# Performance work log

Measured on AMD Instinct MI355X. Metric: run time of the kernel, lower is better.

The kernel has to match this reference:

```python
import jax, jax.numpy as jnp
import numpy as np

B, T, N = 8, 168, 1024
FD, FS, FF = 16, 32, 8
DL, DG, HE, E = 128, 128, 4, 16384
BN = B * N


def _lstm_last(x, Wih, Whh, bih, bhh):
    # x: (BN, T, FD); PyTorch gate order i, f, g, o
    h0 = jnp.zeros((x.shape[0], Whh.shape[1]), x.dtype)
    def step(carry, xt):
        h, c = carry
        g = xt @ Wih.T + h @ Whh.T + bih + bhh
        i, f, gg, o = jnp.split(g, 4, axis=-1)
        c = jax.nn.sigmoid(f) * c + jax.nn.sigmoid(i) * jnp.tanh(gg)
        h = jax.nn.sigmoid(o) * jnp.tanh(c)
        return (h, c), None
    (h, _), _ = jax.lax.scan(step, (h0, h0), jnp.swapaxes(x, 0, 1))
    return h


def _ln(x, g, b):
    mu = x.mean(-1, keepdims=True)
    v = ((x - mu) ** 2).mean(-1, keepdims=True)
    return (x - mu) / jnp.sqrt(v + 1e-5) * g + b


def _gat(x, src, dst, ea, W, a_src, a_dst, a_edge, We, bias):
    # PyG GATConv: concat=False (mean over heads), edge_dim=1, LeakyReLU(0.2)
    xl = (x @ W.T).reshape(BN, HE, -1)                 # (BN, H, C)
    as_ = jnp.sum(xl * a_src, -1)                      # (BN, H)
    ad_ = jnp.sum(xl * a_dst, -1)
    ep = (ea @ We.T).reshape(-1, HE, xl.shape[-1])     # (Eb, H, C)
    ae_ = jnp.sum(ep * a_edge, -1)                     # (Eb, H)
    alpha = jax.nn.leaky_relu(as_[src] + ad_[dst] + ae_, 0.2)
    amax = jax.ops.segment_max(alpha, dst, num_segments=BN)
    ex = jnp.exp(alpha - amax[dst])
    den = jax.ops.segment_sum(ex, dst, num_segments=BN)
    w = ex / den[dst]                                  # softmax over incoming edges
    out = jax.ops.segment_sum(w[:, :, None] * xl[src], dst, num_segments=BN)
    return out.mean(axis=1) + bias


def _forward(fl, edge_index):
    (dyn, fcst, sta, ew,
     lWih, lWhh, lbih, lbhh, sW, sb, fW, fb, uW, ub,
     g0W, g0as, g0ad, g0ae, g0We, g0b,
     g1W, g1as, g1ad, g1ae, g1We, g1b,
     n0g, n0b, n1g, n1b, oW, ob) = fl
    x = jnp.transpose(dyn, (0, 2, 1, 3)).reshape(BN, T, FD)
    z = _lstm_last(x, lWih, lWhh, lbih, lbhh)
    s = jax.nn.relu(sta.reshape(BN, -1) @ sW.T + sb)
    f = jax.nn.relu(fcst.reshape(BN, -1) @ fW.T + fb)
    h = jax.nn.relu(jnp.concatenate([z, s, f], -1) @ uW.T + ub)
    # batch the graph: B disjoint copies with node offsets
    off = (jnp.arange(B) * N)[:, None]
    src = (edge_index[0][None] + off).reshape(-1)
    dst = (edge_index[1][None] + off).reshape(-1)
    ea = jnp.tile(ew.reshape(-1, 1), (B, 1))           # (B*E, 1)
    # PyG GATConv default add_self_loops=True, fill_value='mean' of incoming edge attrs
    deg = jax.ops.segment_sum(jnp.ones_like(ea), dst, num_segments=BN)
    loop_ea = jax.ops.segment_sum(ea, dst, num_segments=BN) / jnp.maximum(deg, 1.0)
    loops = jnp.arange(BN)
    src = jnp.concatenate([src, loops])
    dst = jnp.concatenate([dst, loops])
    ea = jnp.concatenate([ea, loop_ea], 0)
    # hop 0: relu on delta (not last hop), residual (res_proj=None since DL==DG), LayerNorm
    d0 = jax.nn.relu(_gat(h, src, dst, ea, g0W, g0as, g0ad, g0ae, g0We, g0b))
    h = _ln(h + d0, n0g, n0b)
    # hop 1: last hop, no relu on delta
    d1 = _gat(h, src, dst, ea, g1W, g1as, g1ad, g1ae, g1We, g1b)
    h = _ln(h + d1, n1g, n1b)
    return (h @ oW.T + ob).reshape(B, N)


def setup_inputs():
    key = jax.random.key(0)
    ks = iter(jax.random.split(key, 48))
    def rn(shape, s=0.08):
        return jax.random.normal(next(ks), shape, jnp.float32) * s
    HO = HE * DG  # heads * out_channels
    return dict(
        dynamic_features=rn((B, T, N, FD), 1.0),
        forecast_features=rn((B, N, FF), 1.0),
        static_features=rn((B, N, FS), 1.0),
        edge_index=jax.random.randint(next(ks), (2, E), 0, N),
        edge_weight=jax.random.uniform(next(ks), (E,), jnp.float32),
        lstm_Wih=rn((4 * DL, FD)), lstm_Whh=rn((4 * DL, DL)),
        lstm_bih=rn((4 * DL,)), lstm_bhh=rn((4 * DL,)),
        static_W=rn((DL, FS)), static_b=rn((DL,)),
        fcst_W=rn((DL, FF)), fcst_b=rn((DL,)),
        fusion_W=rn((DL, 3 * DL)), fusion_b=rn((DL,)),
        gat0_W=rn((HO, DL)), gat0_att_src=rn((1, HE, DG)), gat0_att_dst=rn((1, HE, DG)),
        gat0_att_edge=rn((1, HE, DG)), gat0_We=rn((HO, 1)), gat0_bias=rn((DG,)),
        gat1_W=rn((HO, DG)), gat1_att_src=rn((1, HE, DG)), gat1_att_dst=rn((1, HE, DG)),
        gat1_att_edge=rn((1, HE, DG)), gat1_We=rn((HO, 1)), gat1_bias=rn((DG,)),
        ln0_g=jnp.ones((DG,), jnp.float32), ln0_b=jnp.zeros((DG,), jnp.float32),
        ln1_g=jnp.ones((DG,), jnp.float32), ln1_b=jnp.zeros((DG,), jnp.float32),
        out_W=rn((1, DG)), out_b=rn((1,)),
    )


def reference(dynamic_features, forecast_features, static_features, edge_weight,
              lstm_Wih, lstm_Whh, lstm_bih, lstm_bhh, static_W, static_b,
              fcst_W, fcst_b, fusion_W, fusion_b,
              gat0_W, gat0_att_src, gat0_att_dst, gat0_att_edge, gat0_We, gat0_bias,
              gat1_W, gat1_att_src, gat1_att_dst, gat1_att_edge, gat1_We, gat1_bias,
              ln0_g, ln0_b, ln1_g, ln1_b, out_W, out_b, edge_index):
    fl = (dynamic_features, forecast_features, static_features, edge_weight,
          lstm_Wih, lstm_Whh, lstm_bih, lstm_bhh, static_W, static_b,
          fcst_W, fcst_b, fusion_W, fusion_b,
          gat0_W, gat0_att_src, gat0_att_dst, gat0_att_edge, gat0_We, gat0_bias,
          gat1_W, gat1_att_src, gat1_att_dst, gat1_att_edge, gat1_We, gat1_bias,
          ln0_g, ln0_b, ln1_g, ln1_b, out_W, out_b)
    return _forward(fl, edge_index)
```

## Files before the change

### kernel.cpp

```cpp
#include <hip/hip_runtime.h>
#include <hip/hip_bf16.h>
#include <stdint.h>

#define BB 8
#define TT 168
#define NN 1024
#define BN_ 8192
#define FD_ 16
#define EE 16384

typedef short short8 __attribute__((ext_vector_type(8)));
typedef __bf16 bf16x8 __attribute__((ext_vector_type(8)));
typedef float f32x4 __attribute__((ext_vector_type(4)));

#if __has_builtin(__builtin_amdgcn_exp2f)
#define EXP2(x) __builtin_amdgcn_exp2f(x)
#else
#define EXP2(x) exp2f(x)
#endif
#if __has_builtin(__builtin_amdgcn_rcpf)
#define RCPF(x) __builtin_amdgcn_rcpf(x)
#else
#define RCPF(x) (1.f / (x))
#endif
#define L2E 1.4426950408889634f
#define T2E 2.8853900817779268f

static __device__ __forceinline__ float b2f(ushort s) {
    unsigned u = ((unsigned)s) << 16;
    return __builtin_bit_cast(float, u);
}
static __device__ __forceinline__ float b2f_lo(unsigned u) {
    return __builtin_bit_cast(float, u << 16);
}
static __device__ __forceinline__ float b2f_hi(unsigned u) {
    return __builtin_bit_cast(float, u & 0xffff0000u);
}
static __device__ __forceinline__ ushort f2b(float f) {
    unsigned u = __builtin_bit_cast(unsigned, f);
    unsigned lsb = (u >> 16) & 1u;
    u += 0x7fffu + lsb;
    return (ushort)(u >> 16);
}
static __device__ __forceinline__ ushort f2b_fast(float f) {
    unsigned u = __builtin_bit_cast(unsigned, f);
    return (ushort)((u + 0x8000u) >> 16);
}
static __device__ __forceinline__ f32x4 mfma16(short8 a, short8 b, f32x4 c) {
    return __builtin_amdgcn_mfma_f32_16x16x32_bf16(
        __builtin_bit_cast(bf16x8, a), __builtin_bit_cast(bf16x8, b), c, 0, 0, 0);
}

#define O_WIH 0
#define O_WHH 8192
#define O_STA 73728
#define O_FCS 335872
#define O_SW  401408
#define O_FW  405504
#define O_UW  406528
#define O_G0W 455680
#define O_G1W 521216
#define O_END 586752

__global__ void cast_kernel(const float* __restrict__ Wih, const float* __restrict__ Whh,
                            const float* __restrict__ sta, const float* __restrict__ fcst,
                            const float* __restrict__ sW, const float* __restrict__ fW,
                            const float* __restrict__ uW, const float* __restrict__ g0W,
                            const float* __restrict__ g1W, ushort* __restrict__ dst) {
    const int i = blockIdx.x * 256 + threadIdx.x;
    if (i >= O_END) return;
    float v;
    if      (i < O_WHH) v = Wih[i - O_WIH];
    else if (i < O_STA) v = Whh[i - O_WHH];
    else if (i < O_FCS) v = sta[i - O_STA];
    else if (i < O_SW)  v = fcst[i - O_FCS];
    else if (i < O_FW)  v = sW[i - O_SW];
    else if (i < O_UW)  v = fW[i - O_FW];
    else if (i < O_G0W) v = uW[i - O_UW];
    else if (i < O_G1W) v = g0W[i - O_G0W];
    else                v = g1W[i - O_G1W];
    dst[i] = f2b(v);
}

__global__ __launch_bounds__(1024) void prep_kernel(
    const int* __restrict__ ei, const float* __restrict__ ew,
    const float* __restrict__ We0, const float* __restrict__ ae0,
    const float* __restrict__ We1, const float* __restrict__ ae1,
    int* __restrict__ deg0, int* __restrict__ offs, float* __restrict__ loopea,
    int* __restrict__ eidx, float* __restrict__ se) {
    __shared__ int degL[1024];
    __shared__ float wsL[1024];
    __shared__ int sc[1024];
    __shared__ float seL[8];
    const int t = threadIdx.x;
    degL[t] = 0; wsL[t] = 0.f;
    if (t < 8) seL[t] = 0.f;
    __syncthreads();
    for (int e = t; e < EE; e += 1024) {
        const int d = ei[EE + e];
        atomicAdd(&degL[d], 1);
        atomicAdd(&wsL[d], ew[e]);
    }
    __syncthreads();
    const int d = degL[t];
    sc[t] = d;
    __syncthreads();
    for (int o = 1; o < 1024; o <<= 1) {
        const int v = (t >= o) ? sc[t - o] : 0;
        __syncthreads();
        sc[t] += v;
        __syncthreads();
    }
    const int excl = sc[t] - d;
    offs[t] = excl;
    deg0[t] = d;
    loopea[t] = wsL[t] / fmaxf((float)d, 1.f);
    degL[t] = excl;
    __syncthreads();
    for (int e = t; e < EE; e += 1024) {
        const int dd = ei[EE + e];
        const int slot = atomicAdd(&degL[dd], 1);
        eidx[slot] = e;
    }
    const int g = t >> 7, k = t & 127;
    const int head = g & 3;
    const float* W = (g >> 2) ? We1 : We0;
    const float* A = (g >> 2) ? ae1 : ae0;
    atomicAdd(&seL[g], W[head * 128 + k] * A[head * 128 + k]);
    __syncthreads();
    if (t < 8) se[t] = seL[t];
}

__global__ __launch_bounds__(256, 2) void lstm_kernel(
    const float* __restrict__ dyn,
    const ushort* __restrict__ Wih,
    const ushort* __restrict__ Whh,
    const float* __restrict__ bih,
    const float* __restrict__ bhh,
    ushort* __restrict__ zsf)
{
    constexpr int HS = 168;
    __shared__ ushort hbuf[2][16 * HS];

    const int tid = threadIdx.x;
    const int blk = blockIdx.x;
    const int b = blk >> 6;
    const int n0 = (blk & 63) << 4;
    const int w = tid >> 6, lane = tid & 63, quad = lane >> 4, m = lane & 15;

    short8 Bf[5][4][2];
    float ci[2], cf[2], cg[2], co[2];
#pragma unroll
    for (int jj = 0; jj < 2; jj++) {
        const int u = (2 * w + jj) * 16 + m;
#pragma unroll
        for (int g = 0; g < 4; g++) {
            const int grow = g * 128 + u;
#pragma unroll
            for (int kt = 0; kt < 4; kt++)
                Bf[kt][g][jj] = *(const short8*)(Whh + grow * 128 + kt * 32 + quad * 8);
            if (quad < 2) Bf[4][g][jj] = *(const short8*)(Wih + grow * 16 + quad * 8);
            else          Bf[4][g][jj] = short8{0, 0, 0, 0, 0, 0, 0, 0};
        }
        ci[jj] = -L2E * (bih[u] + bhh[u]);
        cf[jj] = -L2E * (bih[128 + u] + bhh[128 + u]);
        cg[jj] =  T2E * (bih[256 + u] + bhh[256 + u]);
        co[jj] = -L2E * (bih[384 + u] + bhh[384 + u]);
    }

    float c[2][4];
#pragma unroll
    for (int jj = 0; jj < 2; jj++)
#pragma unroll
        for (int r = 0; r < 4; r++) c[jj][r] = 0.f;

    for (int i = tid; i < 2 * 16 * HS; i += 256) ((ushort*)hbuf)[i] = 0;
    __syncthreads();

    const int xn = tid >> 4, xf = tid & 15;
    const size_t xbase = (size_t)b * TT * NN * FD_ + (size_t)(n0 + xn) * FD_ + xf;
    hbuf[0][xn * HS + 128 + xf] = f2b(dyn[xbase]);
    float xv = dyn[xbase + (size_t)NN * FD_];
    __syncthreads();

    for (int t = 0; t < TT; t++) {
        const ushort* rb = hbuf[t & 1];
        ushort* wb = hbuf[(t + 1) & 1];
        if (t + 1 < TT) wb[xn * HS + 128 + xf] = f2b(xv);
        if (t + 2 < TT) xv = dyn[xbase + (size_t)(t + 2) * NN * FD_];

        f32x4 acc[4][2];
#pragma unroll
        for (int g = 0; g < 4; g++)
#pragma unroll
            for (int jj = 0; jj < 2; jj++) acc[g][jj] = f32x4{0.f, 0.f, 0.f, 0.f};
#pragma unroll
        for (int kt = 0; kt < 5; kt++) {
            short8 a = *(const short8*)&rb[m * HS + kt * 32 + quad * 8];
#pragma unroll
            for (int g = 0; g < 4; g++)
#pragma unroll
                for (int jj = 0; jj < 2; jj++)
                    acc[g][jj] = mfma16(a, Bf[kt][g][jj], acc[g][jj]);
        }

#pragma unroll
        for (int jj = 0; jj < 2; jj++) {
            const int u = (2 * w + jj) * 16 + m;
#pragma unroll
            for (int r = 0; r < 4; r++) {
                const int n = quad * 4 + r;
                const float Di = 1.f + EXP2(fmaf(acc[0][jj][r], -L2E, ci[jj]));
                const float Df = 1.f + EXP2(fmaf(acc[1][jj][r], -L2E, cf[jj]));
                const float Eg = EXP2(fmaf(acc[2][jj][r], T2E, cg[jj]));
                const float Do = 1.f + EXP2(fmaf(acc[3][jj][r], -L2E, co[jj]));
                const float R  = RCPF(Di * (1.f + Eg));
                const float sf = RCPF(Df);
                const float cc = fmaf(sf, c[jj][r], (Eg - 1.f) * R);
                c[jj][r] = cc;
                const float Ec = EXP2(T2E * cc);
                const float h = (Ec - 1.f) * RCPF(Do * (1.f + Ec));
                wb[n * HS + u] = f2b_fast(h);
                if (t == TT - 1) zsf[(size_t)(blk * 16 + n) * 384 + u] = f2b_fast(h);
            }
        }
        __syncthreads();
    }
}

__global__ __launch_bounds__(256) void gemm_sf_kernel(
    const ushort* __restrict__ staB, const ushort* __restrict__ sWB,
    const float* __restrict__ sb,
    const ushort* __restrict__ fcsB, const ushort* __restrict__ fWB,
    const float* __restrict__ fb, ushort* __restrict__ zsf) {
    const int tid = threadIdx.x;
    const int lane = tid & 63, quad = lane >> 4, m = lane & 15;
    int wave = blockIdx.x * 4 + (tid >> 6);
    const short8 z8 = short8{0, 0, 0, 0, 0, 0, 0, 0};
    short8 a, bf;
    int r0, c0, ocol;
    const float* bias;
    if (wave < 4096) {
        r0 = (wave >> 3) * 16; c0 = (wave & 7) * 16; ocol = 128; bias = sb;
        a  = *(const short8*)(staB + (size_t)(r0 + m) * 32 + quad * 8);
        bf = *(const short8*)(sWB + (size_t)(c0 + m) * 32 + quad * 8);
    } else {
        wave -= 4096;
        r0 = (wave >> 3) * 16; c0 = (wave & 7) * 16; ocol = 256; bias = fb;
        a  = (quad == 0) ? *(const short8*)(fcsB + (size_t)(r0 + m) * 8) : z8;
        bf = (quad == 0) ? *(const short8*)(fWB + (size_t)(c0 + m) * 8) : z8;
    }
    f32x4 acc = mfma16(a, bf, f32x4{0.f, 0.f, 0.f, 0.f});
    const float bv = bias[c0 + m];
#pragma unroll
    for (int r = 0; r < 4; r++) {
        const int row = r0 + quad * 4 + r;
        zsf[(size_t)row * 384 + ocol + c0 + m] = f2b(fmaxf(acc[r] + bv, 0.f));
    }
}

__global__ __launch_bounds__(256) void gemm_fusion_kernel(
    const ushort* __restrict__ A, const ushort* __restrict__ Bt,
    const float* __restrict__ bias, ushort* __restrict__ hB, float* __restrict__ hF) {
    const int tid = threadIdx.x;
    const int lane = tid & 63, quad = lane >> 4, m = lane & 15;
    const int wave = blockIdx.x * 4 + (tid >> 6);
    const int r0 = (wave >> 3) * 16, c0 = (wave & 7) * 16;
    f32x4 acc = f32x4{0.f, 0.f, 0.f, 0.f};
#pragma unroll
    for (int kt = 0; kt < 12; kt++) {
        const int k = kt * 32 + quad * 8;
        short8 a  = *(const short8*)(A + (size_t)(r0 + m) * 384 + k);
        short8 bf = *(const short8*)(Bt + (size_t)(c0 + m) * 384 + k);
        acc = mfma16(a, bf, acc);
    }
    const int col = c0 + m;
    const float bv = bias[col];
#pragma unroll
    for (int r = 0; r < 4; r++) {
        const int row = r0 + quad * 4 + r;
        const float v = fmaxf(acc[r] + bv, 0.f);
        hB[(size_t)row * 128 + col] = f2b(v);
        hF[(size_t)row * 128 + col] = v;
    }
}

__global__ __launch_bounds__(256) void gemmatt_kernel(
    const ushort* __restrict__ hB, const ushort* __restrict__ W,
    const float* __restrict__ asrc, const float* __restrict__ adst,
    ushort* __restrict__ xl, float* __restrict__ as_, float* __restrict__ ad_) {
    const int tid = threadIdx.x;
    const int lane = tid & 63, quad = lane >> 4, m = lane & 15;
    const int w = tid >> 6;
    const int r0 = blockIdx.x * 16;
    f32x4 acc[8];
#pragma unroll
    for (int ct = 0; ct < 8; ct++) acc[ct] = f32x4{0.f, 0.f, 0.f, 0.f};
#pragma unroll
    for (int kt = 0; kt < 4; kt++) {
        const int k = kt * 32 + quad * 8;
        short8 a = *(const short8*)(hB + (size_t)(r0 + m) * 128 + k);
#pragma unroll
        for (int ct = 0; ct < 8; ct++) {
            short8 bf = *(const short8*)(W + (size_t)(w * 128 + ct * 16 + m) * 128 + k);
            acc[ct] = mfma16(a, bf, acc[ct]);
        }
    }
    float sa[4] = {0.f, 0.f, 0.f, 0.f}, sd[4] = {0.f, 0.f, 0.f, 0.f};
#pragma unroll
    for (int ct = 0; ct < 8; ct++) {
        const int col = w * 128 + ct * 16 + m;
        const float av = asrc[col], dv = adst[col];
#pragma unroll
        for (int r = 0; r < 4; r++) {
            const float v = acc[ct][r];
            xl[(size_t)(r0 + quad * 4 + r) * 512 + col] = f2b(v);
            sa[r] = fmaf(v, av, sa[r]);
            sd[r] = fmaf(v, dv, sd[r]);
        }
    }
#pragma unroll
    for (int o = 1; o < 16; o <<= 1) {
#pragma unroll
        for (int r = 0; r < 4; r++) {
            sa[r] += __shfl_xor(sa[r], o);
            sd[r] += __shfl_xor(sd[r], o);
        }
    }
    if (m == 0) {
#pragma unroll
        for (int r = 0; r < 4; r++) {
            const int node = r0 + quad * 4 + r;
            as_[node * 4 + w] = sa[r];
            ad_[node * 4 + w] = sd[r];
        }
    }
}

__global__ __launch_bounds__(256) void edge_exp_kernel(
    const int* __restrict__ ei, const float* __restrict__ ew,
    const float* __restrict__ as_, const float* __restrict__ ad_,
    const float* __restrict__ se4, float* __restrict__ pexp) {
    const int idx = blockIdx.x * 256 + threadIdx.x;
    const int b = idx >> 14, e = idx & (EE - 1);
    const int src = b * 1024 + ei[e];
    const int dst = b * 1024 + ei[EE + e];
    const float eaw = ew[e];
    const float4 s4 = *(const float4*)(as_ + src * 4);
    const float4 d4 = *(const float4*)(ad_ + dst * 4);
    float4 p;
    float* pp = (float*)&p;
    const float* s = (const float*)&s4;
    const float* d = (const float*)&d4;
#pragma unroll
    for (int h = 0; h < 4; h++) {
        float a = s[h] + d[h] + eaw * se4[h];
        a = (a < 0.f) ? 0.2f * a : a;
        pp[h] = EXP2(fminf(a, 60.f) * L2E);
    }
    *(float4*)(pexp + (size_t)idx * 4) = p;
}

__global__ __launch_bounds__(256) void gat_kernel(
    float* __restrict__ hF, ushort* __restrict__ hB, const ushort* __restrict__ xl,
    const float* __restrict__ as_, const float* __restrict__ ad_,
    const float* __restrict__ pexp,
    const int* __restrict__ eidx, const int* __restrict__ offs,
    const int* __restrict__ deg0, const float* __restrict__ loopea,
    const int* __restrict__ ei,
    const float* __restrict__ se4, const float* __restrict__ bias,
    const float* __restrict__ lng, const float* __restrict__ lnb, int relu,
    int writeOut, const float* __restrict__ oW, const float* __restrict__ ob,
    float* __restrict__ out) {
    const int lane = threadIdx.x & 63;
    const int half = lane >> 5;
    const int c0 = (lane & 31) * 2;
    const int v = blockIdx.x * 4 + (threadIdx.x >> 6);
    const int b = v >> 10, n = v & 1023;
    const int dg = deg0[n], off = offs[n];

    const float lea = loopea[n];
    const float4 s4 = *(const float4*)(as_ + v * 4);
    const float4 d4 = *(const float4*)(ad_ + v * 4);
    const float* sp = (const float*)&s4;
    const float* dp = (const float*)&d4;
    float den[4], num[4][4];
#pragma unroll
    for (int h = 0; h < 4; h++) {
        float a = sp[h] + dp[h] + lea * se4[h];
        a = (a < 0.f) ? 0.2f * a : a;
        float p = EXP2(fminf(a, 60.f) * L2E);
        if (half) p = 0.f;
        den[h] = p;
        const unsigned xa = *(const unsigned*)(xl + (size_t)v * 512 + h * 128 + c0);
        const unsigned xb = *(const unsigned*)(xl + (size_t)v * 512 + h * 128 + 64 + c0);
        num[h][0] = p * b2f_lo(xa);
        num[h][1] = p * b2f_hi(xa);
        num[h][2] = p * b2f_lo(xb);
        num[h][3] = p * b2f_hi(xb);
    }
    for (int i = half; i < dg; i += 2) {
        const int e = eidx[off + i];
        const int src = b * 1024 + ei[e];
        const float4 p4 = *(const float4*)(pexp + (size_t)(b * EE + e) * 4);
        const float* p = (const float*)&p4;
        const ushort* xr = xl + (size_t)src * 512 + c0;
#pragma unroll
        for (int h = 0; h < 4; h++) {
            const unsigned xa = *(const unsigned*)(xr + h * 128);
            const unsigned xb = *(const unsigned*)(xr + h * 128 + 64);
            den[h] += p[h];
            num[h][0] = fmaf(p[h], b2f_lo(xa), num[h][0]);
            num[h][1] = fmaf(p[h], b2f_hi(xa), num[h][1]);
            num[h][2] = fmaf(p[h], b2f_lo(xb), num[h][2]);
            num[h][3] = fmaf(p[h], b2f_hi(xb), num[h][3]);
        }
    }
#pragma unroll
    for (int h = 0; h < 4; h++) {
        den[h] += __shfl_xor(den[h], 32);
#pragma unroll
        for (int k = 0; k < 4; k++) num[h][k] += __shfl_xor(num[h][k], 32);
    }

    float o[4] = {0.f, 0.f, 0.f, 0.f};
#pragma unroll
    for (int h = 0; h < 4; h++) {
        const float inv = RCPF(den[h]);
#pragma unroll
        for (int k = 0; k < 4; k++) o[k] = fmaf(num[h][k], inv, o[k]);
    }

    const float2 bva = *(const float2*)(bias + c0);
    const float2 bvb = *(const float2*)(bias + 64 + c0);
    float d0 = o[0] * 0.25f + bva.x;
    float d1 = o[1] * 0.25f + bva.y;
    float d2 = o[2] * 0.25f + bvb.x;
    float d3 = o[3] * 0.25f + bvb.y;
    if (relu) {
        d0 = fmaxf(d0, 0.f); d1 = fmaxf(d1, 0.f);
        d2 = fmaxf(d2, 0.f); d3 = fmaxf(d3, 0.f);
    }
    const float2 hva = *(const float2*)(hF + (size_t)v * 128 + c0);
    const float2 hvb = *(const float2*)(hF + (size_t)v * 128 + 64 + c0);
    const float x0 = hva.x + d0, x1 = hva.y + d1;
    const float x2 = hvb.x + d2, x3 = hvb.y + d3;

    float s = (x0 + x1) + (x2 + x3);
#pragma unroll
    for (int o2 = 32; o2; o2 >>= 1) s += __shfl_xor(s, o2);
    const float mu = s * (1.f / 256.f);
    const float e0 = x0 - mu, e1 = x1 - mu, e2 = x2 - mu, e3 = x3 - mu;
    float vs = (e0 * e0 + e1 * e1) + (e2 * e2 + e3 * e3);
#pragma unroll
    for (int o2 = 32; o2; o2 >>= 1) vs += __shfl_xor(vs, o2);
    const float r = rsqrtf(vs * (1.f / 256.f) + 1e-5f);
    const float2 lga = *(const float2*)(lng + c0);
    const float2 lgb = *(const float2*)(lng + 64 + c0);
    const float2 lba = *(const float2*)(lnb + c0);
    const float2 lbb = *(const float2*)(lnb + 64 + c0);
    const float y0 = e0 * r * lga.x + lba.x;
    const float y1 = e1 * r * lga.y + lba.y;
    const float y2 = e2 * r * lgb.x + lbb.x;
    const float y3 = e3 * r * lgb.y + lbb.y;
    if (writeOut) {
        const float2 owa = *(const float2*)(oW + c0);
        const float2 owb = *(const float2*)(oW + 64 + c0);
        float t = (y0 * owa.x + y1 * owa.y) + (y2 * owb.x + y3 * owb.y);
#pragma unroll
        for (int o2 = 32; o2; o2 >>= 1) t += __shfl_xor(t, o2);
        if (lane == 0) out[v] = t * 0.5f + ob[0];
    } else if (half == 0) {
        *(float2*)(hF + (size_t)v * 128 + c0) = float2{y0, y1};
        *(float2*)(hF + (size_t)v * 128 + 64 + c0) = float2{y2, y3};
        const unsigned pka = (unsigned)f2b(y0) | ((unsigned)f2b(y1) << 16);
        const unsigned pkb = (unsigned)f2b(y2) | ((unsigned)f2b(y3) << 16);
        *(unsigned*)(hB + (size_t)v * 128 + c0) = pka;
        *(unsigned*)(hB + (size_t)v * 128 + 64 + c0) = pkb;
    }
}

extern "C" void kernel_launch(void* const* d_in, const int* in_sizes, int n_in,
                              void* d_out, int out_size, void* d_ws, size_t ws_size,
                              hipStream_t stream) {
    const float* dyn  = (const float*)d_in[0];
    const float* fcst = (const float*)d_in[1];
    const float* sta  = (const float*)d_in[2];
    const int*   ei   = (const int*)d_in[3];
    const float* ew   = (const float*)d_in[4];
    const float* lWih = (const float*)d_in[5];
    const float* lWhh = (const float*)d_in[6];
    const float* lbih = (const float*)d_in[7];
    const float* lbhh = (const float*)d_in[8];
    const float* sW = (const float*)d_in[9];
    const float* sb = (const float*)d_in[10];
    const float* fW = (const float*)d_in[11];
    const float* fb = (const float*)d_in[12];
    const float* uW = (const float*)d_in[13];
    const float* ub = (const float*)d_in[14];
    const float* g0W  = (const float*)d_in[15];
    const float* g0as = (const float*)d_in[16];
    const float* g0ad = (const float*)d_in[17];
    const float* g0ae = (const float*)d_in[18];
    const float* g0We = (const float*)d_in[19];
    const float* g0b  = (const float*)d_in[20];
    const float* g1W  = (const float*)d_in[21];
    const float* g1as = (const float*)d_in[22];
    const float* g1ad = (const float*)d_in[23];
    const float* g1ae = (const float*)d_in[24];
    const float* g1We = (const float*)d_in[25];
    const float* g1b  = (const float*)d_in[26];
    const float* ln0g = (const float*)d_in[27];
    const float* ln0b = (const float*)d_in[28];
    const float* ln1g = (const float*)d_in[29];
    const float* ln1b = (const float*)d_in[30];
    const float* oW = (const float*)d_in[31];
    const float* ob = (const float*)d_in[32];

    char* p = (char*)d_ws;
    ushort* castB = (ushort*)p; p += (size_t)O_END * 2 + 512;
    ushort* zsf = (ushort*)p;  p += (size_t)BN_ * 384 * 2;
    float*  hF  = (float*)p;   p += (size_t)BN_ * 128 * 4;
    ushort* hB  = (ushort*)p;  p += (size_t)BN_ * 128 * 2;
    ushort* xl  = (ushort*)p;  p += (size_t)BN_ * 512 * 2;
    float*  asb = (float*)p;   p += (size_t)BN_ * 4 * 4;
    float*  adb = (float*)p;   p += (size_t)BN_ * 4 * 4;
    int*    deg0   = (int*)p;   p += 4096;
    int*    offs   = (int*)p;   p += 4096;
    float*  loopea = (float*)p; p += 4096;
    int*    eidx   = (int*)p;   p += (size_t)EE * 4;
    float*  se     = (float*)p; p += 256;
    float*  pexp   = (float*)zsf;

    const ushort* WihB = castB + O_WIH;
    const ushort* WhhB = castB + O_WHH;
    const ushort* staB = castB + O_STA;
    const ushort* fcsB = castB + O_FCS;
    const ushort* sWB  = castB + O_SW;
    const ushort* fWB  = castB + O_FW;
    const ushort* uWB  = castB + O_UW;
    const ushort* g0WB = castB + O_G0W;
    const ushort* g1WB = castB + O_G1W;

    cast_kernel<<<(O_END + 255) / 256, 256, 0, stream>>>(lWih, lWhh, sta, fcst, sW, fW,
                                                         uW, g0W, g1W, castB);
    prep_kernel<<<1, 1024, 0, stream>>>(ei, ew, g0We, g0ae, g1We, g1ae,
                                        deg0, offs, loopea, eidx, se);

    lstm_kernel<<<512, 256, 0, stream>>>(dyn, WihB, WhhB, lbih, lbhh, zsf);
    gemm_sf_kernel<<<2048, 256, 0, stream>>>(staB, sWB, sb, fcsB, fWB, fb, zsf);
    gemm_fusion_kernel<<<1024, 256, 0, stream>>>(zsf, uWB, ub, hB, hF);

    gemmatt_kernel<<<512, 256, 0, stream>>>(hB, g0WB, g0as, g0ad, xl, asb, adb);
    edge_exp_kernel<<<512, 256, 0, stream>>>(ei, ew, asb, adb, se, pexp);
    gat_kernel<<<2048, 256, 0, stream>>>(hF, hB, xl, asb, adb, pexp, eidx, offs, deg0,
                                         loopea, ei, se, g0b, ln0g, ln0b, 1,
                                         0, oW, ob, (float*)d_out);
    gemmatt_kernel<<<512, 256, 0, stream>>>(hB, g1WB, g1as, g1ad, xl, asb, adb);
    edge_exp_kernel<<<512, 256, 0, stream>>>(ei, ew, asb, adb, se + 4, pexp);
    gat_kernel<<<2048, 256, 0, stream>>>(hF, hB, xl, asb, adb, pexp, eidx, offs, deg0,
                                         loopea, ei, se + 4, g1b, ln1g, ln1b, 0,
                                         1, oW, ob, (float*)d_out);
}
```

Before: 556.9 us.

## Fuse cast with prep kernel and fold static/forecast GEMMs into fusion GEMM

The weight cast kernel and the single-block edge prep kernel are merged into one launch, with block 0 doing prep and the remaining blocks casting. The static and forecast projection GEMMs now run inside the fusion GEMM: each block computes its 16 rows of those features into shared memory and reads them directly as A operands. This removes two launches and the global round trip for the static/forecast part of the concatenated input. In exchange, each block now covers 16 rows with 8 waves and needs a barrier.

```diff
diff --git a/kernel.cpp b/kernel.cpp
--- a/kernel.cpp
+++ b/kernel.cpp
@@ -62,32 +62,33 @@
 #define O_G1W 521216
 #define O_END 586752
 
-__global__ void cast_kernel(const float* __restrict__ Wih, const float* __restrict__ Whh,
-                            const float* __restrict__ sta, const float* __restrict__ fcst,
-                            const float* __restrict__ sW, const float* __restrict__ fW,
-                            const float* __restrict__ uW, const float* __restrict__ g0W,
-                            const float* __restrict__ g1W, ushort* __restrict__ dst) {
-    const int i = blockIdx.x * 256 + threadIdx.x;
-    if (i >= O_END) return;
-    float v;
-    if      (i < O_WHH) v = Wih[i - O_WIH];
-    else if (i < O_STA) v = Whh[i - O_WHH];
-    else if (i < O_FCS) v = sta[i - O_STA];
-    else if (i < O_SW)  v = fcst[i - O_FCS];
-    else if (i < O_FW)  v = sW[i - O_SW];
-    else if (i < O_UW)  v = fW[i - O_FW];
-    else if (i < O_G0W) v = uW[i - O_UW];
-    else if (i < O_G1W) v = g0W[i - O_G0W];
-    else                v = g1W[i - O_G1W];
-    dst[i] = f2b(v);
-}
-
-__global__ __launch_bounds__(1024) void prep_kernel(
+__global__ __launch_bounds__(1024) void cast_prep_kernel(
+    const float* __restrict__ Wih, const float* __restrict__ Whh,
+    const float* __restrict__ sta, const float* __restrict__ fcst,
+    const float* __restrict__ sW, const float* __restrict__ fW,
+    const float* __restrict__ uW, const float* __restrict__ g0W,
+    const float* __restrict__ g1W, ushort* __restrict__ dst,
     const int* __restrict__ ei, const float* __restrict__ ew,
     const float* __restrict__ We0, const float* __restrict__ ae0,
     const float* __restrict__ We1, const float* __restrict__ ae1,
     int* __restrict__ deg0, int* __restrict__ offs, float* __restrict__ loopea,
     int* __restrict__ eidx, float* __restrict__ se) {
+    if (blockIdx.x != 0) {
+        const int i = (blockIdx.x - 1) * 1024 + threadIdx.x;
+        if (i >= O_END) return;
+        float v;
+        if      (i < O_WHH) v = Wih[i - O_WIH];
+        else if (i < O_STA) v = Whh[i - O_WHH];
+        else if (i < O_FCS) v = sta[i - O_STA];
+        else if (i < O_SW)  v = fcst[i - O_FCS];
+        else if (i < O_FW)  v = sW[i - O_SW];
+        else if (i < O_UW)  v = fW[i - O_FW];
+        else if (i < O_G0W) v = uW[i - O_UW];
+        else if (i < O_G1W) v = g0W[i - O_G0W];
+        else                v = g1W[i - O_G1W];
+        dst[i] = f2b(v);
+        return;
+    }
     __shared__ int degL[1024];
     __shared__ float wsL[1024];
     __shared__ int sc[1024];
@@ -228,51 +229,46 @@
     }
 }
 
-__global__ __launch_bounds__(256) void gemm_sf_kernel(
+__global__ __launch_bounds__(512) void gemm_fusion_kernel(
     const ushort* __restrict__ staB, const ushort* __restrict__ sWB,
     const float* __restrict__ sb,
     const ushort* __restrict__ fcsB, const ushort* __restrict__ fWB,
-    const float* __restrict__ fb, ushort* __restrict__ zsf) {
+    const float* __restrict__ fb,
+    const ushort* __restrict__ zsfA, const ushort* __restrict__ Bt,
+    const float* __restrict__ bias, ushort* __restrict__ hB, float* __restrict__ hF) {
+    constexpr int LP = 264;
+    __shared__ ushort sf[16][LP];
     const int tid = threadIdx.x;
     const int lane = tid & 63, quad = lane >> 4, m = lane & 15;
-    int wave = blockIdx.x * 4 + (tid >> 6);
+    const int w = tid >> 6;
+    const int r0 = blockIdx.x * 16, c0 = w * 16;
     const short8 z8 = short8{0, 0, 0, 0, 0, 0, 0, 0};
-    short8 a, bf;
-    int r0, c0, ocol;
-    const float* bias;
-    if (wave < 4096) {
-        r0 = (wave >> 3) * 16; c0 = (wave & 7) * 16; ocol = 128; bias = sb;
-        a  = *(const short8*)(staB + (size_t)(r0 + m) * 32 + quad * 8);
-        bf = *(const short8*)(sWB + (size_t)(c0 + m) * 32 + quad * 8);
-    } else {
-        wave -= 4096;
-        r0 = (wave >> 3) * 16; c0 = (wave & 7) * 16; ocol = 256; bias = fb;
-        a  = (quad == 0) ? *(const short8*)(fcsB + (size_t)(r0 + m) * 8) : z8;
-        bf = (quad == 0) ? *(const short8*)(fWB + (size_t)(c0 + m) * 8) : z8;
-    }
-    f32x4 acc = mfma16(a, bf, f32x4{0.f, 0.f, 0.f, 0.f});
-    const float bv = bias[c0 + m];
+
+    short8 a = *(const short8*)(staB + (size_t)(r0 + m) * 32 + quad * 8);
+    short8 bf = *(const short8*)(sWB + (size_t)(c0 + m) * 32 + quad * 8);
+    f32x4 acc_s = mfma16(a, bf, f32x4{0.f, 0.f, 0.f, 0.f});
+    a  = (quad == 0) ? *(const short8*)(fcsB + (size_t)(r0 + m) * 8) : z8;
+    bf = (quad == 0) ? *(const short8*)(fWB + (size_t)(c0 + m) * 8) : z8;
+    f32x4 acc_f = mfma16(a, bf, f32x4{0.f, 0.f, 0.f, 0.f});
+
+    const float sbv = sb[c0 + m], fbv = fb[c0 + m];
 #pragma unroll
     for (int r = 0; r < 4; r++) {
-        const int row = r0 + quad * 4 + r;
-        zsf[(size_t)row * 384 + ocol + c0 + m] = f2b(fmaxf(acc[r] + bv, 0.f));
-    }
-}
-
-__global__ __launch_bounds__(256) void gemm_fusion_kernel(
-    const ushort* __restrict__ A, const ushort* __restrict__ Bt,
-    const float* __restrict__ bias, ushort* __restrict__ hB, float* __restrict__ hF) {
-    const int tid = threadIdx.x;
-    const int lane = tid & 63, quad = lane >> 4, m = lane & 15;
-    const int wave = blockIdx.x * 4 + (tid >> 6);
-    const int r0 = (wave >> 3) * 16, c0 = (wave & 7) * 16;
+        const int row = quad * 4 + r;
+        sf[row][c0 + m]       = f2b(fmaxf(acc_s[r] + sbv, 0.f));
+        sf[row][128 + c0 + m] = f2b(fmaxf(acc_f[r] + fbv, 0.f));
+    }
+    __syncthreads();
+
     f32x4 acc = f32x4{0.f, 0.f, 0.f, 0.f};
 #pragma unroll
     for (int kt = 0; kt < 12; kt++) {
         const int k = kt * 32 + quad * 8;
-        short8 a  = *(const short8*)(A + (size_t)(r0 + m) * 384 + k);
-        short8 bf = *(const short8*)(Bt + (size_t)(c0 + m) * 384 + k);
-        acc = mfma16(a, bf, acc);
+        short8 av;
+        if (kt < 4) av = *(const short8*)(zsfA + (size_t)(r0 + m) * 384 + k);
+        else        av = *(const short8*)&sf[m][k - 128];
+        short8 bv = *(const short8*)(Bt + (size_t)(c0 + m) * 384 + k);
+        acc = mfma16(av, bv, acc);
     }
     const int col = c0 + m;
     const float bv = bias[col];
@@ -542,14 +538,13 @@
     const ushort* g0WB = castB + O_G0W;
     const ushort* g1WB = castB + O_G1W;
 
-    cast_kernel<<<(O_END + 255) / 256, 256, 0, stream>>>(lWih, lWhh, sta, fcst, sW, fW,
-                                                         uW, g0W, g1W, castB);
-    prep_kernel<<<1, 1024, 0, stream>>>(ei, ew, g0We, g0ae, g1We, g1ae,
-                                        deg0, offs, loopea, eidx, se);
+    cast_prep_kernel<<<1 + (O_END + 1023) / 1024, 1024, 0, stream>>>(
+        lWih, lWhh, sta, fcst, sW, fW, uW, g0W, g1W, castB,
+        ei, ew, g0We, g0ae, g1We, g1ae, deg0, offs, loopea, eidx, se);
 
     lstm_kernel<<<512, 256, 0, stream>>>(dyn, WihB, WhhB, lbih, lbhh, zsf);
-    gemm_sf_kernel<<<2048, 256, 0, stream>>>(staB, sWB, sb, fcsB, fWB, fb, zsf);
-    gemm_fusion_kernel<<<1024, 256, 0, stream>>>(zsf, uWB, ub, hB, hF);
+    gemm_fusion_kernel<<<512, 512, 0, stream>>>(staB, sWB, sb, fcsB, fWB, fb,
+                                                zsf, uWB, ub, hB, hF);
 
     gemmatt_kernel<<<512, 256, 0, stream>>>(hB, g0WB, g0as, g0ad, xl, asb, adb);
     edge_exp_kernel<<<512, 256, 0, stream>>>(ei, ew, asb, adb, se, pexp);
```

New measurement: 550.2 us. No clear change (-1.2%).
